# Performance work log

Hardware: AMD Instinct MI355X
Metric: run time of the kernel (lower is better)

## Reference

```python
import jax, jax.numpy as jnp
import numpy as np

K = 9  # 3x3 kernel field

def _conv(x, w, b, pad):
    out = jax.lax.conv_general_dilated(x, w, (1, 1), ((pad, pad), (pad, pad)),
                                       dimension_numbers=('NCHW', 'OIHW', 'NCHW'))
    return out + b[None, :, None, None]

def _conv_transpose(x, w, b):
    # torch ConvTranspose2d(k=3, stride=2, padding=1, output_padding=1); w: [Cin, Cout, 3, 3]
    wk = jnp.flip(jnp.transpose(w, (1, 0, 2, 3)), axis=(2, 3))  # [Cout, Cin, 3, 3]
    out = jax.lax.conv_general_dilated(x, wk, (1, 1), ((1, 2), (1, 2)),
                                       lhs_dilation=(2, 2),
                                       dimension_numbers=('NCHW', 'OIHW', 'NCHW'))
    return out + b[None, :, None, None]

def _modulated_deform_conv(x, offset, mask, w, b):
    # x: [B,C,H,W], offset: [B,2K,H,W] (y,x interleaved per kernel point, row-major),
    # mask: [B,K,H,W], w: [O,C,3,3]; stride=1, pad=1, dilation=1
    B, C, H, W = x.shape
    O = w.shape[0]
    off = offset.reshape(B, K, 2, H, W)
    ky, kx = jnp.meshgrid(jnp.arange(3), jnp.arange(3), indexing='ij')
    base_y = (jnp.arange(H)[None, :, None] - 1 + ky.reshape(K, 1, 1)).astype(x.dtype)  # [K,H,1]
    base_x = (jnp.arange(W)[None, None, :] - 1 + kx.reshape(K, 1, 1)).astype(x.dtype)  # [K,1,W]
    py = off[:, :, 0] + base_y[None]  # [B,K,H,W]
    px = off[:, :, 1] + base_x[None]
    y0 = jnp.floor(py); x0 = jnp.floor(px)
    wy = py - y0; wx = px - x0
    y0i = y0.astype(jnp.int32); x0i = x0.astype(jnp.int32)
    flat = x.reshape(B, C, H * W)

    def gather(yi, xi):
        valid = ((yi >= 0) & (yi < H) & (xi >= 0) & (xi < W)).astype(x.dtype)
        idx = jnp.clip(yi, 0, H - 1) * W + jnp.clip(xi, 0, W - 1)  # [B,K,H,W]
        g = jax.vmap(lambda im, ix: im[:, ix])(flat, idx.reshape(B, -1))  # [B,C,K*H*W]
        return g.reshape(B, C, K, H, W) * valid[:, None]

    v = (gather(y0i, x0i)         * ((1 - wy) * (1 - wx))[:, None]
       + gather(y0i, x0i + 1)     * ((1 - wy) * wx)[:, None]
       + gather(y0i + 1, x0i)     * (wy * (1 - wx))[:, None]
       + gather(y0i + 1, x0i + 1) * (wy * wx)[:, None])
    v = v * mask[:, None]  # modulation
    out = jnp.einsum('bckhw,ock->bohw', v, w.reshape(O, C, K))
    return out + b[None, :, None, None]

def setup_inputs() -> dict:
    key = jax.random.key(0)
    ks = jax.random.split(key, 8)
    B, Cin, Cout, H, W = 4, 128, 64, 64, 64
    return {
        'high_feature': jax.random.normal(ks[0], (B, Cin, H, W), jnp.float32),
        'low_feature': jax.random.normal(ks[1], (B, Cout, 2 * H, 2 * W), jnp.float32),
        'w_up': jax.random.normal(ks[2], (Cin, Cout, 3, 3), jnp.float32) * 0.03,
        'b_up': jnp.zeros((Cout,), jnp.float32),
        'w_off': jax.random.normal(ks[3], (3 * K, 2 * Cout, 3, 3), jnp.float32) * 0.02,
        'b_off': jnp.zeros((3 * K,), jnp.float32),
        'w_align': jax.random.normal(ks[4], (Cout, Cout, 3, 3), jnp.float32) * 0.04,
        'b_align': jnp.zeros((Cout,), jnp.float32),
    }

def reference(high_feature, low_feature, w_up, b_up, w_off, b_off, w_align, b_align):
    up = _conv_transpose(high_feature, w_up, b_up)            # [B,Cout,2H,2W]
    fo = _conv(jnp.concatenate([up, low_feature], axis=1), w_off, b_off, 1)
    offset, mask = fo[:, :2 * K], fo[:, 2 * K:]
    mask = 2.0 * jax.nn.sigmoid(mask)
    aligned = _modulated_deform_conv(up, offset, mask, w_align, b_align)
    aligned = jnp.where(aligned >= 0, aligned, 0.2 * aligned)  # LeakyReLU(0.2)
    return jnp.concatenate([aligned, low_feature], axis=1)
```

## Files before the change

kernel.cpp:

```cpp
#include <hip/hip_runtime.h>
#include <math.h>

namespace {
constexpr int B   = 4;
constexpr int CIN = 128;
constexpr int CO  = 64;
constexpr int HF  = 64;
constexpr int HO  = 128;
constexpr int HW  = HO * HO;
constexpr int NOFF = 27;

constexpr size_t UPB  = 0;
constexpr size_t LOB  = UPB + (size_t)B * HW * CO / 2;
constexpr size_t HBF  = LOB + (size_t)B * HW * CO / 2;
constexpr size_t WFRG = HBF + (size_t)B * HF * HF * CIN / 2;
constexpr size_t WFUP = WFRG + (size_t)(4 * 18 * 64 * 8) / 2;
constexpr size_t WFOF = WFUP + (size_t)(9 * 4 * 4 * 64 * 8) / 2;
}

using short8 = __attribute__((ext_vector_type(8))) short;
using f32x4  = __attribute__((ext_vector_type(4))) float;

__device__ __forceinline__ unsigned short f2bf(float f) {
  unsigned u = __float_as_uint(f);
  u += 0x7fffu + ((u >> 16) & 1u);
  return (unsigned short)(u >> 16);
}

__global__ __launch_bounds__(256) void k_prep(const float* __restrict__ high,
                                              const float* __restrict__ low,
                                              const float* __restrict__ wup,
                                              const float* __restrict__ woff,
                                              const float* __restrict__ wal,
                                              float* __restrict__ out,
                                              float* __restrict__ ws) {
  __shared__ unsigned short tl[64][130];
  const int bid = blockIdx.x;
  const int t = threadIdx.x;

  if (bid < 288) {
    int i = bid * 256 + t;
    if (i < 4 * 18 * 64 * 8) {
      int j = i & 7; int t2 = i >> 3;
      int lane = t2 & 63; int t3 = t2 >> 6;
      int kb = t3 % 18; int w = t3 / 18;
      int tap = kb >> 1;
      int c = (kb & 1) * 32 + ((lane >> 4) << 3) + j;
      int o = (w << 4) + (lane & 15);
      unsigned short* wfrag = (unsigned short*)(ws + WFRG);
      wfrag[i] = f2bf(wal[((size_t)o * CO + c) * 9 + tap]);
    }
    if (i < 9 * 4 * 4 * 64 * 8) {
      int j = i & 7; int lane = (i >> 3) & 63; int w = (i >> 9) & 3;
      int ch = (i >> 11) & 3; int rr = i >> 13;
      int c = ch * 32 + ((lane >> 4) << 3) + j;
      int o = w * 16 + (lane & 15);
      unsigned short* wfup = (unsigned short*)(ws + WFUP);
      wfup[i] = f2bf(wup[((size_t)c * CO + o) * 9 + rr]);
    }
    if (i < 9 * 4 * 2 * 64 * 8) {
      int j = i & 7; int lane = (i >> 3) & 63; int nt = (i >> 9) & 1;
      int kc = (i >> 10) & 3; int tap = i >> 12;
      int c = kc * 32 + ((lane >> 4) << 3) + j;
      int o = nt * 16 + (lane & 15);
      float v = 0.f;
      if (o < NOFF) v = woff[(((size_t)o * 2 * CO + c) * 3 + tap / 3) * 3 + (tap % 3)];
      unsigned short* wfo = (unsigned short*)(ws + WFOF);
      wfo[i] = f2bf(v);
    }
    return;
  }

  if (bid < 544) {
    unsigned short (*tl2)[66] = (unsigned short(*)[66])&tl[0][0];
    unsigned short* hbf = (unsigned short*)(ws + HBF);
    int j = bid - 288;
    const int y = j & 63, b = j >> 6;
    const int x = t & 63, clb = t >> 6;
    for (int c0 = 0; c0 < CIN; c0 += 32) {
      __syncthreads();
#pragma unroll
      for (int k = 0; k < 8; ++k) {
        int cl = clb * 8 + k;
        float v = high[(((size_t)b * CIN + c0 + cl) * HF + y) * HF + x];
        tl2[cl][x] = f2bf(v);
      }
      __syncthreads();
      int px = t >> 2, cg = t & 3;
      ushort4 a, bb;
      a.x = tl2[cg * 8 + 0][px]; a.y = tl2[cg * 8 + 1][px];
      a.z = tl2[cg * 8 + 2][px]; a.w = tl2[cg * 8 + 3][px];
      bb.x = tl2[cg * 8 + 4][px]; bb.y = tl2[cg * 8 + 5][px];
      bb.z = tl2[cg * 8 + 6][px]; bb.w = tl2[cg * 8 + 7][px];
      unsigned short* dst = hbf + (((size_t)b * HF + y) * HF + px) * CIN + c0 + cg * 8;
      *(ushort4*)(dst) = a;
      *(ushort4*)(dst + 4) = bb;
    }
    return;
  }

  {
    unsigned short* lob = (unsigned short*)(ws + LOB);
    int j = bid - 544;
    const int y = j & 127, b = j >> 7;
#pragma unroll
    for (int it = 0; it < 8; ++it) {
      int i = it * 256 + t;
      int c = i >> 5, xi = (i & 31) * 4;
      float4 v = *(const float4*)(low + (((size_t)b * CO + c) * HO + y) * HO + xi);
      *(float4*)(out + (((size_t)b * 2 * CO + CO + c) * HO + y) * HO + xi) = v;
      tl[c][xi + 0] = f2bf(v.x); tl[c][xi + 1] = f2bf(v.y);
      tl[c][xi + 2] = f2bf(v.z); tl[c][xi + 3] = f2bf(v.w);
    }
    __syncthreads();
#pragma unroll
    for (int it = 0; it < 4; ++it) {
      int i = it * 256 + t;
      int x = i >> 3, cg = i & 7;
      unsigned rw[4];
#pragma unroll
      for (int p = 0; p < 4; ++p)
        rw[p] = (unsigned)tl[cg * 8 + 2 * p][x] | ((unsigned)tl[cg * 8 + 2 * p + 1][x] << 16);
      *(uint4*)(lob + (((size_t)b * HO + y) * HO + x) * CO + cg * 8) =
          make_uint4(rw[0], rw[1], rw[2], rw[3]);
    }
  }
}

union SmemUp {
  unsigned short At[2][4][85][8];
  float accs[4][16][65];
};

__global__ __launch_bounds__(256) void k_up(const float* __restrict__ bup,
                                            float* __restrict__ ws) {
  __shared__ SmemUp sm;
  const unsigned short* hbf = (const unsigned short*)(ws + HBF);
  const uint4* wfu = (const uint4*)(ws + WFUP);
  unsigned short* upb = (unsigned short*)(ws + UPB);

  const int t    = threadIdx.x;
  const int lane = t & 63;
  const int oq   = __builtin_amdgcn_readfirstlane(t >> 6);
  const int orig = blockIdx.x;
  const int tile = ((orig & 7) << 7) + (orig >> 3);
  const int par  = tile & 3;
  const int pyv  = (par >> 1) & 1, pxv = par & 1;
  const int tx   = ((tile >> 2) & 3) * 16;
  const int ty   = ((tile >> 4) & 15) * 4;
  const int b    = tile >> 8;
  const int nty  = pyv + 1, ntx = pxv + 1;

  uint4 s0, s1;
  const int pxA = t >> 2, cgA = t & 3;
  const int i2 = t + 256, pxB = i2 >> 2, cgB = i2 & 3;

  auto load_chunk = [&](int c0) {
    {
      int gy = ty + pxA / 17, gx = tx + pxA % 17;
      s0 = make_uint4(0, 0, 0, 0);
      if (gy < HF && gx < HF)
        s0 = *(const uint4*)(hbf + (((size_t)b * HF + gy) * HF + gx) * CIN + c0 + cgA * 8);
    }
    s1 = make_uint4(0, 0, 0, 0);
    if (pxB < 85) {
      int gy = ty + pxB / 17, gx = tx + pxB % 17;
      if (gy < HF && gx < HF)
        s1 = *(const uint4*)(hbf + (((size_t)b * HF + gy) * HF + gx) * CIN + c0 + cgB * 8);
    }
  };
  auto write_chunk = [&](int buf) {
    *(uint4*)&sm.At[buf][cgA][pxA][0] = s0;
    if (pxB < 85) *(uint4*)&sm.At[buf][cgB][pxB][0] = s1;
  };

  f32x4 acc[4];
#pragma unroll
  for (int mt = 0; mt < 4; ++mt) acc[mt] = {0.f, 0.f, 0.f, 0.f};

  load_chunk(0);
  write_chunk(0);
  __syncthreads();

  union Cvt { uint4 u; short8 s; };
  int buf = 0;
#pragma unroll 1
  for (int ch = 0; ch < 4; ++ch) {
    if (ch < 3) load_chunk((ch + 1) * 32);
#pragma unroll
    for (int ti = 0; ti < 2; ++ti) {
      if (ti < nty) {
#pragma unroll
        for (int tj = 0; tj < 2; ++tj) {
          if (tj < ntx) {
            int ryA = pyv ? 2 - 2 * ti : 1;
            int rxA = pxv ? 2 - 2 * tj : 1;
            int rr = ryA * 3 + rxA;
            Cvt bw; bw.u = wfu[(((size_t)rr * 4 + ch) * 4 + oq) * 64 + lane];
#pragma unroll
            for (int mt = 0; mt < 4; ++mt) {
              Cvt av;
              av.u = *(const uint4*)&sm.At[buf][lane >> 4][(mt + ti) * 17 + (lane & 15) + tj][0];
              acc[mt] = __builtin_amdgcn_mfma_f32_16x16x32_bf16(av.s, bw.s, acc[mt], 0, 0, 0);
            }
          }
        }
      }
    }
    if (ch < 3) write_chunk(buf ^ 1);
    __syncthreads();
    buf ^= 1;
  }

#pragma unroll
  for (int mt = 0; mt < 4; ++mt)
#pragma unroll
    for (int r = 0; r < 4; ++r)
      sm.accs[oq][lane & 15][mt * 16 + (lane >> 4) * 4 + r] = acc[mt][r];
  __syncthreads();

  const int yo = 2 * (ty + (lane >> 4)) + pyv;
  const int xo = 2 * (tx + (lane & 15)) + pxv;
  unsigned short* dst = upb + (((size_t)b * HO + yo) * HO + xo) * CO + oq * 16;
  unsigned rw[8];
#pragma unroll
  for (int p = 0; p < 8; ++p) {
    float v0 = sm.accs[oq][2 * p][lane] + bup[oq * 16 + 2 * p];
    float v1 = sm.accs[oq][2 * p + 1][lane] + bup[oq * 16 + 2 * p + 1];
    rw[p] = (unsigned)f2bf(v0) | ((unsigned)f2bf(v1) << 16);
  }
  *(uint4*)dst = make_uint4(rw[0], rw[1], rw[2], rw[3]);
  *(uint4*)(dst + 8) = make_uint4(rw[4], rw[5], rw[6], rw[7]);
}

__global__ __launch_bounds__(256) void k_offdcn(const float* __restrict__ boff,
                                                const float* __restrict__ bal,
                                                float* __restrict__ out,
                                                const float* __restrict__ ws) {
  __shared__ float smem[7936];
  unsigned short* us_in = (unsigned short*)smem;
  float* fo_raw = smem;
  unsigned* prm = (unsigned*)(smem + 2112);
  unsigned short* us_vt = (unsigned short*)(smem + 3840);

  const unsigned short* upb = (const unsigned short*)(ws + UPB);
  const unsigned short* lob = (const unsigned short*)(ws + LOB);
  const uint4* wfo = (const uint4*)(ws + WFOF);
  const uint4* wf  = (const uint4*)(ws + WFRG);

  const int t = threadIdx.x;
  const int lane = t & 63;
  const int w = __builtin_amdgcn_readfirstlane(t >> 6);
  const int mh = w >> 1, nt = w & 1;
  const int oq = w;
  const int orig = blockIdx.x;
  const int tile = ((orig & 7) << 7) + (orig >> 3);
  const int tX = (tile & 7) * 16;
  const int tY = ((tile >> 3) & 31) * 4;
  const int b  = tile >> 8;
  const unsigned short* upB = upb + (size_t)b * HW * CO;

  union Cvt { uint4 u; short8 s; };

  for (int i = t; i < 16 * 108; i += 256) {
    int px = i >> 4, cg = i & 15;
    int gy = tY - 1 + px / 18, gx = tX - 1 + px % 18;
    uint4 v = make_uint4(0, 0, 0, 0);
    if (gy >= 0 && gy < HO && gx >= 0 && gx < HO) {
      const unsigned short* src =
          (cg < 8 ? upb : lob) + (((size_t)b * HO + gy) * HO + gx) * CO + (cg & 7) * 8;
      v = *(const uint4*)src;
    }
    *(uint4*)&us_in[((size_t)cg * 108 + px) * 8] = v;
  }
  __syncthreads();

  f32x4 acc2[2];
  acc2[0] = {0.f, 0.f, 0.f, 0.f}; acc2[1] = {0.f, 0.f, 0.f, 0.f};
#pragma unroll 1
  for (int tap = 0; tap < 9; ++tap) {
    int ky = tap / 3, kx = tap % 3;
#pragma unroll
    for (int kc = 0; kc < 4; ++kc) {
      Cvt bw; bw.u = wfo[(((size_t)tap * 4 + kc) * 2 + nt) * 64 + lane];
#pragma unroll
      for (int mt = 0; mt < 2; ++mt) {
        int sy = mh * 2 + mt;
        Cvt av;
        av.u = *(const uint4*)&us_in[(((size_t)(kc * 4 + (lane >> 4))) * 108 +
                                      (sy + ky) * 18 + (lane & 15) + kx) * 8];
        acc2[mt] = __builtin_amdgcn_mfma_f32_16x16x32_bf16(av.s, bw.s, acc2[mt], 0, 0, 0);
      }
    }
  }
  __syncthreads();

#pragma unroll
  for (int mt = 0; mt < 2; ++mt)
#pragma unroll
    for (int r = 0; r < 4; ++r)
      fo_raw[(nt * 16 + (lane & 15)) * 66 + mh * 32 + mt * 16 + (lane >> 4) * 4 + r] =
          acc2[mt][r];
  __syncthreads();

  for (int i = t; i < 9 * 64; i += 256) {
    int k = i >> 6, px = i & 63;
    int y = tY + (px >> 4), x = tX + (px & 15);
    float offy = fo_raw[(2 * k) * 66 + px] + boff[2 * k];
    float offx = fo_raw[(2 * k + 1) * 66 + px] + boff[2 * k + 1];
    float m = 2.f / (1.f + expf(-(fo_raw[(18 + k) * 66 + px] + boff[18 + k])));
    float pyf = offy + (float)(y - 1 + k / 3);
    float pxf = offx + (float)(x - 1 + k % 3);
    float y0f = floorf(pyf), x0f = floorf(pxf);
    float wy = pyf - y0f, wx = pxf - x0f;
    int y0 = (int)y0f, x0 = (int)x0f;
    int y1 = y0 + 1, x1 = x0 + 1;
    float vy0 = (y0 >= 0 && y0 < HO) ? m : 0.f;
    float vy1 = (y1 >= 0 && y1 < HO) ? m : 0.f;
    float vx0 = (x0 >= 0 && x0 < HO) ? 1.f : 0.f;
    float vx1 = (x1 >= 0 && x1 < HO) ? 1.f : 0.f;
    float w0 = (1.f - wy) * (1.f - wx) * vy0 * vx0;
    float w1 = (1.f - wy) * wx * vy0 * vx1;
    float w2 = wy * (1.f - wx) * vy1 * vx0;
    float w3 = wy * wx * vy1 * vx1;
    int cy0 = min(max(y0, 0), HO - 1), cy1 = min(max(y1, 0), HO - 1);
    int cx0 = min(max(x0, 0), HO - 1), cx1 = min(max(x1, 0), HO - 1);
    unsigned pc = (unsigned)cy0 | ((unsigned)cy1 << 8) |
                  ((unsigned)cx0 << 16) | ((unsigned)cx1 << 24);
    unsigned* pr = prm + ((size_t)k * 64 + px) * 3;
    pr[0] = (unsigned)f2bf(w0) | ((unsigned)f2bf(w1) << 16);
    pr[1] = (unsigned)f2bf(w2) | ((unsigned)f2bf(w3) << 16);
    pr[2] = pc;
  }
  __syncthreads();

  uint4 u00[2], u01[2], u10[2], u11[2];

  auto issue = [&](int k) {
#pragma unroll
    for (int it = 0; it < 2; ++it) {
      int j = it * 256 + t;
      int q = j & 7, px = j >> 3;
      unsigned pc = prm[((size_t)k * 64 + px) * 3 + 2];
      int cy0 = pc & 255, cy1 = (pc >> 8) & 255, cx0 = (pc >> 16) & 255, cx1 = pc >> 24;
      const unsigned short* base = upB + q * 8;
      u00[it] = *(const uint4*)(base + (size_t)(cy0 * HO + cx0) * CO);
      u01[it] = *(const uint4*)(base + (size_t)(cy0 * HO + cx1) * CO);
      u10[it] = *(const uint4*)(base + (size_t)(cy1 * HO + cx0) * CO);
      u11[it] = *(const uint4*)(base + (size_t)(cy1 * HO + cx1) * CO);
    }
  };

  auto combine = [&](int k, int buf) {
#pragma unroll
    for (int it = 0; it < 2; ++it) {
      int j = it * 256 + t;
      int q = j & 7, px = j >> 3;
      const unsigned* pr = prm + ((size_t)k * 64 + px) * 3;
      unsigned pw01 = pr[0], pw23 = pr[1];
      float w0 = __uint_as_float(pw01 << 16), w1 = __uint_as_float(pw01 & 0xffff0000u);
      float w2 = __uint_as_float(pw23 << 16), w3 = __uint_as_float(pw23 & 0xffff0000u);
      unsigned a0[4] = {u00[it].x, u00[it].y, u00[it].z, u00[it].w};
      unsigned a1[4] = {u01[it].x, u01[it].y, u01[it].z, u01[it].w};
      unsigned a2[4] = {u10[it].x, u10[it].y, u10[it].z, u10[it].w};
      unsigned a3[4] = {u11[it].x, u11[it].y, u11[it].z, u11[it].w};
      unsigned rw[4];
#pragma unroll
      for (int p = 0; p < 4; ++p) {
        float l0 = __uint_as_float(a0[p] << 16), h0 = __uint_as_float(a0[p] & 0xffff0000u);
        float l1 = __uint_as_float(a1[p] << 16), h1 = __uint_as_float(a1[p] & 0xffff0000u);
        float l2 = __uint_as_float(a2[p] << 16), h2 = __uint_as_float(a2[p] & 0xffff0000u);
        float l3 = __uint_as_float(a3[p] << 16), h3 = __uint_as_float(a3[p] & 0xffff0000u);
        float vlo = fmaf(w0, l0, fmaf(w1, l1, fmaf(w2, l2, w3 * l3)));
        float vhi = fmaf(w0, h0, fmaf(w1, h1, fmaf(w2, h2, w3 * h3)));
        rw[p] = (unsigned)f2bf(vlo) | ((unsigned)f2bf(vhi) << 16);
      }
      *(uint4*)&us_vt[(((size_t)buf * 8 + q) * 64 + px) * 8] = make_uint4(rw[0], rw[1], rw[2], rw[3]);
    }
  };

  f32x4 acc[4];
#pragma unroll
  for (int mt = 0; mt < 4; ++mt) acc[mt] = {0.f, 0.f, 0.f, 0.f};

  uint4 bw0 = wf[(oq * 18 + 0) * 64 + lane];
  uint4 bw1 = wf[(oq * 18 + 1) * 64 + lane];
  uint4 bn0, bn1;

  issue(0);
  combine(0, 0);
  __syncthreads();

  int buf = 0;
#pragma unroll 1
  for (int k = 0; k < 9; ++k) {
    if (k < 8) {
      issue(k + 1);
      bn0 = wf[(oq * 18 + 2 * k + 2) * 64 + lane];
      bn1 = wf[(oq * 18 + 2 * k + 3) * 64 + lane];
    }
#pragma unroll
    for (int kb2 = 0; kb2 < 2; ++kb2) {
      Cvt bfr; bfr.u = kb2 ? bw1 : bw0;
#pragma unroll
      for (int mt = 0; mt < 4; ++mt) {
        Cvt av;
        av.u = *(const uint4*)&us_vt[(((size_t)buf * 8 + kb2 * 4 + (lane >> 4)) * 64 +
                                      mt * 16 + (lane & 15)) * 8];
        acc[mt] = __builtin_amdgcn_mfma_f32_16x16x32_bf16(av.s, bfr.s, acc[mt], 0, 0, 0);
      }
    }
    if (k < 8) combine(k + 1, buf ^ 1);
    __syncthreads();
    bw0 = bn0; bw1 = bn1;
    buf ^= 1;
  }

  float* accs = smem;
#pragma unroll
  for (int mt = 0; mt < 4; ++mt)
#pragma unroll
    for (int r = 0; r < 4; ++r)
      accs[((size_t)oq * 16 + (lane & 15)) * 65 + mt * 16 + (lane >> 4) * 4 + r] = acc[mt][r];
  __syncthreads();

  const int y = tY + (lane >> 4), x = tX + (lane & 15);
  float* ob = out + (size_t)b * 2 * CO * HW + (size_t)y * HO + x;
#pragma unroll
  for (int ol = 0; ol < 16; ++ol) {
    int o = oq * 16 + ol;
    float v = accs[((size_t)oq * 16 + ol) * 65 + lane] + bal[o];
    v = (v >= 0.f) ? v : 0.2f * v;
    ob[(size_t)o * HW] = v;
  }
}

extern "C" void kernel_launch(void* const* d_in, const int* in_sizes, int n_in,
                              void* d_out, int out_size, void* d_ws, size_t ws_size,
                              hipStream_t stream) {
  const float* high = (const float*)d_in[0];
  const float* low  = (const float*)d_in[1];
  const float* wup  = (const float*)d_in[2];
  const float* bup  = (const float*)d_in[3];
  const float* woff = (const float*)d_in[4];
  const float* boff = (const float*)d_in[5];
  const float* wal  = (const float*)d_in[6];
  const float* bal  = (const float*)d_in[7];
  float* out = (float*)d_out;
  float* ws  = (float*)d_ws;

  k_prep<<<dim3(1056), dim3(256), 0, stream>>>(high, low, wup, woff, wal, out, ws);
  k_up<<<dim3(1024), dim3(256), 0, stream>>>(bup, ws);
  k_offdcn<<<dim3(1024), dim3(256), 0, stream>>>(boff, bal, out, ws);
}
```

Baseline: 64.23 us.

## Compute all four parity phases per block in k_up and deepen offdcn gather prefetch

k_up now has each block compute all four output parity phases for its input tile instead of one, so the staged input tile in shared memory is loaded once and reused four times, and the grid drops from 1024 to 256 blocks. This cuts redundant global reads of the high feature but quadruples accumulator registers and reduces the number of blocks, which may hurt occupancy and load balance. In k_offdcn the gather issue is moved one iteration further ahead, placed after combine, to better hide gather latency behind the MFMA work.

```diff
diff --git a/kernel.cpp b/kernel.cpp
--- a/kernel.cpp
+++ b/kernel.cpp
@@ -143,13 +143,10 @@
   const int lane = t & 63;
   const int oq   = __builtin_amdgcn_readfirstlane(t >> 6);
   const int orig = blockIdx.x;
-  const int tile = ((orig & 7) << 7) + (orig >> 3);
-  const int par  = tile & 3;
-  const int pyv  = (par >> 1) & 1, pxv = par & 1;
-  const int tx   = ((tile >> 2) & 3) * 16;
-  const int ty   = ((tile >> 4) & 15) * 4;
-  const int b    = tile >> 8;
-  const int nty  = pyv + 1, ntx = pxv + 1;
+  const int tile = ((orig & 7) << 5) + (orig >> 3);
+  const int tx   = (tile & 3) * 16;
+  const int ty   = ((tile >> 2) & 15) * 4;
+  const int b    = tile >> 6;
 
   uint4 s0, s1;
   const int pxA = t >> 2, cgA = t & 3;
@@ -174,9 +171,11 @@
     if (pxB < 85) *(uint4*)&sm.At[buf][cgB][pxB][0] = s1;
   };
 
-  f32x4 acc[4];
-#pragma unroll
-  for (int mt = 0; mt < 4; ++mt) acc[mt] = {0.f, 0.f, 0.f, 0.f};
+  f32x4 acc[4][4];
+#pragma unroll
+  for (int p = 0; p < 4; ++p)
+#pragma unroll
+    for (int mt = 0; mt < 4; ++mt) acc[p][mt] = {0.f, 0.f, 0.f, 0.f};
 
   load_chunk(0);
   write_chunk(0);
@@ -188,20 +187,25 @@
   for (int ch = 0; ch < 4; ++ch) {
     if (ch < 3) load_chunk((ch + 1) * 32);
 #pragma unroll
-    for (int ti = 0; ti < 2; ++ti) {
-      if (ti < nty) {
-#pragma unroll
-        for (int tj = 0; tj < 2; ++tj) {
-          if (tj < ntx) {
-            int ryA = pyv ? 2 - 2 * ti : 1;
-            int rxA = pxv ? 2 - 2 * tj : 1;
-            int rr = ryA * 3 + rxA;
-            Cvt bw; bw.u = wfu[(((size_t)rr * 4 + ch) * 4 + oq) * 64 + lane];
-#pragma unroll
-            for (int mt = 0; mt < 4; ++mt) {
-              Cvt av;
-              av.u = *(const uint4*)&sm.At[buf][lane >> 4][(mt + ti) * 17 + (lane & 15) + tj][0];
-              acc[mt] = __builtin_amdgcn_mfma_f32_16x16x32_bf16(av.s, bw.s, acc[mt], 0, 0, 0);
+    for (int par = 0; par < 4; ++par) {
+      const int pyv = par >> 1, pxv = par & 1;
+#pragma unroll
+      for (int ti = 0; ti < 2; ++ti) {
+        if (ti <= pyv) {
+#pragma unroll
+          for (int tj = 0; tj < 2; ++tj) {
+            if (tj <= pxv) {
+              int ryA = pyv ? 2 - 2 * ti : 1;
+              int rxA = pxv ? 2 - 2 * tj : 1;
+              int rr = ryA * 3 + rxA;
+              Cvt bw; bw.u = wfu[(((size_t)rr * 4 + ch) * 4 + oq) * 64 + lane];
+#pragma unroll
+              for (int mt = 0; mt < 4; ++mt) {
+                Cvt av;
+                av.u = *(const uint4*)&sm.At[buf][lane >> 4][(mt + ti) * 17 + (lane & 15) + tj][0];
+                acc[par][mt] =
+                    __builtin_amdgcn_mfma_f32_16x16x32_bf16(av.s, bw.s, acc[par][mt], 0, 0, 0);
+              }
             }
           }
         }
@@ -212,25 +216,30 @@
     buf ^= 1;
   }
 
-#pragma unroll
-  for (int mt = 0; mt < 4; ++mt)
-#pragma unroll
-    for (int r = 0; r < 4; ++r)
-      sm.accs[oq][lane & 15][mt * 16 + (lane >> 4) * 4 + r] = acc[mt][r];
-  __syncthreads();
-
-  const int yo = 2 * (ty + (lane >> 4)) + pyv;
-  const int xo = 2 * (tx + (lane & 15)) + pxv;
-  unsigned short* dst = upb + (((size_t)b * HO + yo) * HO + xo) * CO + oq * 16;
-  unsigned rw[8];
-#pragma unroll
-  for (int p = 0; p < 8; ++p) {
-    float v0 = sm.accs[oq][2 * p][lane] + bup[oq * 16 + 2 * p];
-    float v1 = sm.accs[oq][2 * p + 1][lane] + bup[oq * 16 + 2 * p + 1];
-    rw[p] = (unsigned)f2bf(v0) | ((unsigned)f2bf(v1) << 16);
-  }
-  *(uint4*)dst = make_uint4(rw[0], rw[1], rw[2], rw[3]);
-  *(uint4*)(dst + 8) = make_uint4(rw[4], rw[5], rw[6], rw[7]);
+#pragma unroll 1
+  for (int par = 0; par < 4; ++par) {
+    const int pyv = par >> 1, pxv = par & 1;
+#pragma unroll
+    for (int mt = 0; mt < 4; ++mt)
+#pragma unroll
+      for (int r = 0; r < 4; ++r)
+        sm.accs[oq][lane & 15][mt * 16 + (lane >> 4) * 4 + r] = acc[par][mt][r];
+    __syncthreads();
+
+    const int yo = 2 * (ty + (lane >> 4)) + pyv;
+    const int xo = 2 * (tx + (lane & 15)) + pxv;
+    unsigned short* dst = upb + (((size_t)b * HO + yo) * HO + xo) * CO + oq * 16;
+    unsigned rw[8];
+#pragma unroll
+    for (int p = 0; p < 8; ++p) {
+      float v0 = sm.accs[oq][2 * p][lane] + bup[oq * 16 + 2 * p];
+      float v1 = sm.accs[oq][2 * p + 1][lane] + bup[oq * 16 + 2 * p + 1];
+      rw[p] = (unsigned)f2bf(v0) | ((unsigned)f2bf(v1) << 16);
+    }
+    *(uint4*)dst = make_uint4(rw[0], rw[1], rw[2], rw[3]);
+    *(uint4*)(dst + 8) = make_uint4(rw[4], rw[5], rw[6], rw[7]);
+    __syncthreads();
+  }
 }
 
 __global__ __launch_bounds__(256) void k_offdcn(const float* __restrict__ boff,
@@ -389,16 +398,12 @@
 
   issue(0);
   combine(0, 0);
+  issue(1);
   __syncthreads();
 
   int buf = 0;
 #pragma unroll 1
   for (int k = 0; k < 9; ++k) {
-    if (k < 8) {
-      issue(k + 1);
-      bn0 = wf[(oq * 18 + 2 * k + 2) * 64 + lane];
-      bn1 = wf[(oq * 18 + 2 * k + 3) * 64 + lane];
-    }
 #pragma unroll
     for (int kb2 = 0; kb2 < 2; ++kb2) {
       Cvt bfr; bfr.u = kb2 ? bw1 : bw0;
@@ -410,7 +415,12 @@
         acc[mt] = __builtin_amdgcn_mfma_f32_16x16x32_bf16(av.s, bfr.s, acc[mt], 0, 0, 0);
       }
     }
-    if (k < 8) combine(k + 1, buf ^ 1);
+    if (k < 8) {
+      combine(k + 1, buf ^ 1);
+      if (k < 7) issue(k + 2);
+      bn0 = wf[(oq * 18 + 2 * k + 2) * 64 + lane];
+      bn1 = wf[(oq * 18 + 2 * k + 3) * 64 + lane];
+    }
     __syncthreads();
     bw0 = bn0; bw1 = bn1;
     buf ^= 1;
@@ -450,6 +460,6 @@
   float* ws  = (float*)d_ws;
 
   k_prep<<<dim3(1056), dim3(256), 0, stream>>>(high, low, wup, woff, wal, out, ws);
-  k_up<<<dim3(1024), dim3(256), 0, stream>>>(bup, ws);
+  k_up<<<dim3(256), dim3(256), 0, stream>>>(bup, ws);
   k_offdcn<<<dim3(1024), dim3(256), 0, stream>>>(boff, bal, out, ws);
 }
```

After: 73.21 us. +14.0%, slower.
